# Performance work log

Measured on AMD Instinct MI355X. Metric: run time of the kernel, lower is better.

The kernel has to match this reference:

```python
import jax, jax.numpy as jnp
import numpy as np

B, S, D, H = 4, 2048, 512, 8
HD = D // H  # head_dim = 64


def setup_inputs() -> dict:
    key = jax.random.key(0)
    ks = jax.random.split(key, 6)
    s = 1.0 / np.sqrt(D)
    return {
        "value": jax.random.normal(ks[0], (B, S, D), jnp.float32),
        "key": jax.random.normal(ks[1], (B, S, D), jnp.float32),
        "query": jax.random.normal(ks[2], (B, S, D), jnp.float32),
        "Wv": jax.random.normal(ks[3], (D, D), jnp.float32) * s,
        "bv": jnp.zeros((D,), jnp.float32),
        "Wk": jax.random.normal(ks[4], (D, D), jnp.float32) * s,
        "bk": jnp.zeros((D,), jnp.float32),
        "Wq": jax.random.normal(ks[5], (D, D), jnp.float32) * s,
        "bq": jnp.zeros((D,), jnp.float32),
    }


def _heads(x):
    # [B,S,D] -> [B,H,S,hd]
    return x.reshape(B, S, H, HD).transpose(0, 2, 1, 3)


def reference(value, key, query, Wv, bv, Wk, bk, Wq, bq):
    v = _heads(value @ Wv.T + bv)
    k = _heads(key @ Wk.T + bk)
    q = _heads(query @ Wq.T + bq)
    scale = 1.0 / jnp.sqrt(jnp.asarray(HD, q.dtype))
    # two scaled-dot-product score maps, each [B,H,S,S]
    att_kq = jax.nn.softmax(jnp.einsum("bhqd,bhkd->bhqk", q, k) * scale, axis=-1)
    att_vq = jax.nn.softmax(jnp.einsum("bhqd,bhkd->bhqk", q, v) * scale, axis=-1)
    att_map = att_kq + att_vq
    fused = v + k  # [B,H,S,hd]
    attended = jnp.einsum("bhqk,bhkd->bhqd", att_map, fused)
    # elementwise multiply with q, reduce over the sequence (query) axis
    head_logits = jnp.sum(attended * q, axis=2)  # [B,H,hd]
    return head_logits.reshape(B, H * HD)
```

## Files before the change

kernel.cpp:

```cpp
#include <hip/hip_runtime.h>
#include <hip/hip_bf16.h>

#define Bq 4
#define Sq 2048
#define Dq 512
#define Hq 8
#define HDq 64

typedef __attribute__((ext_vector_type(8))) short short8;
typedef __attribute__((ext_vector_type(4))) float f32x4;

#if __has_builtin(__builtin_amdgcn_exp2f)
#define EXP2(x) __builtin_amdgcn_exp2f(x)
#else
#define EXP2(x) exp2f(x)
#endif

#define SCALE2 (0.125f * 1.44269504088896340736f)
#define INV_SCALE2 (5.545177444479562f)

__device__ __forceinline__ short bfs(float x) {
    __hip_bfloat16 h = __float2bfloat16(x);
    short r;
    __builtin_memcpy(&r, &h, 2);
    return r;
}

__device__ __forceinline__ short8 cvt8(float4 a, float4 b) {
    union { __hip_bfloat16 h[8]; short8 s; } u;
    u.h[0] = __float2bfloat16(a.x); u.h[1] = __float2bfloat16(a.y);
    u.h[2] = __float2bfloat16(a.z); u.h[3] = __float2bfloat16(a.w);
    u.h[4] = __float2bfloat16(b.x); u.h[5] = __float2bfloat16(b.y);
    u.h[6] = __float2bfloat16(b.z); u.h[7] = __float2bfloat16(b.w);
    return u.s;
}

__device__ __forceinline__ void gload16(const void* g, void* l) {
    __builtin_amdgcn_global_load_lds(
        (const __attribute__((address_space(1))) unsigned int*)g,
        (__attribute__((address_space(3))) unsigned int*)l, 16, 0, 0);
}

__global__ __launch_bounds__(256, 3)
void proj_kernel(const float* __restrict__ Xv, const float* __restrict__ Xk, const float* __restrict__ Xq,
                 const float* __restrict__ Wv, const float* __restrict__ Wk, const float* __restrict__ Wq,
                 const float* __restrict__ bv, const float* __restrict__ bk, const float* __restrict__ bq,
                 __hip_bfloat16* __restrict__ Ov, __hip_bfloat16* __restrict__ Ok, __hip_bfloat16* __restrict__ Oq) {
    __shared__ alignas(16) short As[128 * 64];
    __shared__ alignas(16) short Bs[128 * 64];

    const int z = blockIdx.z;
    const float* X   = (z == 0) ? Xv : (z == 1) ? Xk : Xq;
    const float* W   = (z == 0) ? Wv : (z == 1) ? Wk : Wq;
    const float* bia = (z == 0) ? bv : (z == 1) ? bk : bq;
    __hip_bfloat16* O = (z == 0) ? Ov : (z == 1) ? Ok : Oq;
    const float sc = (z == 2) ? SCALE2 : 1.0f;

    const int tid  = threadIdx.x;
    const int lane = tid & 63;
    const int w    = tid >> 6;
    const int wr   = w >> 1;
    const int wc   = w & 1;
    const int m0   = blockIdx.y * 128;
    const int n0   = blockIdx.x * 128;
    const int arow = lane & 15;
    const int ag   = lane >> 4;

    f32x4 acc[4][4];
    #pragma unroll
    for (int t = 0; t < 4; ++t)
        #pragma unroll
        for (int u = 0; u < 4; ++u) acc[t][u] = (f32x4){0.f, 0.f, 0.f, 0.f};

    for (int kk = 0; kk < Dq / 64; ++kk) {
        __syncthreads();
        #pragma unroll
        for (int p = 0; p < 4; ++p) {
            int id  = p * 256 + tid;
            int row = id >> 3;
            int c   = id & 7;
            int dst = row * 128 + ((c * 16) ^ ((row & 7) << 4));
            const float* ax = X + (size_t)(m0 + row) * Dq + kk * 64 + c * 8;
            const float* bx = W + (size_t)(n0 + row) * Dq + kk * 64 + c * 8;
            float4 a0 = *(const float4*)ax;
            float4 a1 = *(const float4*)(ax + 4);
            float4 b0 = *(const float4*)bx;
            float4 b1 = *(const float4*)(bx + 4);
            *(short8*)((char*)As + dst) = cvt8(a0, a1);
            *(short8*)((char*)Bs + dst) = cvt8(b0, b1);
        }
        __syncthreads();
        #pragma unroll
        for (int h = 0; h < 2; ++h) {
            short8 af[4], bf[4];
            #pragma unroll
            for (int t = 0; t < 4; ++t) {
                int ra = wr * 64 + t * 16 + arow;
                int rb = wc * 64 + t * 16 + arow;
                af[t] = *(const short8*)((const char*)As + ra * 128 + ((h * 64 + ag * 16) ^ ((ra & 7) << 4)));
                bf[t] = *(const short8*)((const char*)Bs + rb * 128 + ((h * 64 + ag * 16) ^ ((rb & 7) << 4)));
            }
            #pragma unroll
            for (int t = 0; t < 4; ++t)
                #pragma unroll
                for (int u = 0; u < 4; ++u)
                    acc[t][u] = __builtin_amdgcn_mfma_f32_16x16x32_bf16(af[t], bf[u], acc[t][u], 0, 0, 0);
        }
    }

    float biasv[4];
    #pragma unroll
    for (int u = 0; u < 4; ++u) biasv[u] = bia[n0 + wc * 64 + u * 16 + arow];

    #pragma unroll
    for (int t = 0; t < 4; ++t) {
        #pragma unroll
        for (int u = 0; u < 4; ++u) {
            #pragma unroll
            for (int r = 0; r < 4; ++r) {
                int m = m0 + wr * 64 + t * 16 + 4 * ag + r;
                int n = n0 + wc * 64 + u * 16 + arow;
                int b = m >> 11, s = m & 2047;
                int hh = n >> 6, hd = n & 63;
                O[((((size_t)b * Hq + hh) * Sq + s) << 6) + hd] =
                    __float2bfloat16((acc[t][u][r] + biasv[u]) * sc);
            }
        }
    }
}

__global__ __launch_bounds__(256)
void fuse_t_kernel(const __hip_bfloat16* __restrict__ Kh, const __hip_bfloat16* __restrict__ Vh,
                   __hip_bfloat16* __restrict__ Ft) {
    __shared__ float T[64][65];
    const int bh = blockIdx.x >> 5;
    const int st = blockIdx.x & 31;
    const int tid = threadIdx.x;

    #pragma unroll
    for (int p = 0; p < 2; ++p) {
        int idx = p * 256 + tid;
        int r = idx >> 3;
        int c = (idx & 7) * 8;
        size_t g = ((size_t)bh * Sq + st * 64 + r) * 64 + c;
        float4 k4 = *(const float4*)((const char*)Kh + g * 2);
        float4 v4 = *(const float4*)((const char*)Vh + g * 2);
        const __hip_bfloat16* kp = (const __hip_bfloat16*)&k4;
        const __hip_bfloat16* vp = (const __hip_bfloat16*)&v4;
        #pragma unroll
        for (int j = 0; j < 8; ++j)
            T[r][c + j] = __bfloat162float(kp[j]) + __bfloat162float(vp[j]);
    }
    __syncthreads();
    #pragma unroll
    for (int pp = 0; pp < 2; ++pp) {
        int idx = pp * 256 + tid;
        int d  = idx >> 3;
        int p8 = (idx & 7) * 8;
        alignas(16) __hip_bfloat16 tmp[8];
        #pragma unroll
        for (int j2 = 0; j2 < 8; ++j2) {
            int p = p8 + j2;
            int h  = p >> 5;
            int ag = (p >> 3) & 3;
            int j  = p & 7;
            int k  = 16 * (2 * (j >> 2) + h) + 4 * ag + (j & 3);
            tmp[j2] = __float2bfloat16(T[k][d]);
        }
        *(float4*)((char*)Ft + (((size_t)bh * 64 + d) * Sq + st * 64 + p8) * 2) = *(const float4*)tmp;
    }
}

__global__ __launch_bounds__(512, 4)
void attn_kernel(const __hip_bfloat16* __restrict__ Qh, const __hip_bfloat16* __restrict__ Kh,
                 const __hip_bfloat16* __restrict__ Vh, const __hip_bfloat16* __restrict__ Ft,
                 float* __restrict__ part) {
    __shared__ alignas(16) short Qs[128 * 64];
    __shared__ alignas(16) short Ks[64 * 64];
    __shared__ alignas(16) short Vs[64 * 64];
    __shared__ alignas(16) short Fs[64 * 64];
    __shared__ float part_s[8][64];

    const int tid  = threadIdx.x;
    const int lane = tid & 63;
    const int w    = tid >> 6;
    const int lb   = (blockIdx.x & 7) * 64 + (blockIdx.x >> 3);
    const int bh   = lb >> 4;
    const int s0   = (lb & 15) * 128;

    const char* Qbh = (const char*)(Qh + (size_t)bh * Sq * 64);
    const char* Kbh = (const char*)(Kh + (size_t)bh * Sq * 64);
    const char* Vbh = (const char*)(Vh + (size_t)bh * Sq * 64);
    const char* Fbh = (const char*)(Ft + (size_t)bh * 64 * Sq);

    #pragma unroll
    for (int p = 0; p < 2; ++p) {
        int idx = p * 512 + tid;
        int r = idx >> 3;
        int c = idx & 7;
        int swz = (r & 7) << 4;
        float4 q4 = *(const float4*)(Qbh + ((size_t)(s0 + r) * 64 + c * 8) * 2);
        *(float4*)((char*)Qs + r * 128 + ((c * 16) ^ swz)) = q4;
    }
    __syncthreads();

    const int arow = lane & 15;
    const int ag   = lane >> 4;
    const int aswz = (arow & 7) << 4;

    const int qrow = w * 16 + arow;
    short8 qa0 = *(const short8*)((const char*)Qs + qrow * 128 + ((16 * ag) ^ aswz));
    short8 qa1 = *(const short8*)((const char*)Qs + qrow * 128 + ((64 + 16 * ag) ^ aswz));

    f32x4 acc_k[4], acc_v[4];
    #pragma unroll
    for (int t = 0; t < 4; ++t) {
        acc_k[t] = (f32x4){0.f, 0.f, 0.f, 0.f};
        acc_v[t] = (f32x4){0.f, 0.f, 0.f, 0.f};
    }
    float lp_k = 0.f, lp_v = 0.f;

    const int sgr = w * 8 + (lane >> 3);
    const int scs = (lane & 7) ^ (sgr & 7);
    const size_t koff = ((size_t)sgr * 64 + scs * 8) * 2;
    char* ldsK = (char*)Ks + w * 1024;
    char* ldsV = (char*)Vs + w * 1024;
    char* ldsF = (char*)Fs + w * 1024;

    for (int ck = 0; ck < Sq / 64; ++ck) {
        const int kv0 = ck * 64;
        __syncthreads();
        gload16(Kbh + (size_t)kv0 * 128 + koff, ldsK);
        gload16(Vbh + (size_t)kv0 * 128 + koff, ldsV);
        gload16(Fbh + ((size_t)sgr * Sq + kv0 + scs * 8) * 2, ldsF);
        __syncthreads();

        f32x4 sk[4], sv[4];
        #pragma unroll
        for (int t = 0; t < 4; ++t) {
            sk[t] = (f32x4){0.f, 0.f, 0.f, 0.f};
            sv[t] = (f32x4){0.f, 0.f, 0.f, 0.f};
        }
        #pragma unroll
        for (int t = 0; t < 4; ++t) {
            int brow = t * 16 + arow;
            int bswz = (brow & 7) << 4;
            short8 kb0 = *(const short8*)((const char*)Ks + brow * 128 + ((16 * ag) ^ bswz));
            short8 kb1 = *(const short8*)((const char*)Ks + brow * 128 + ((64 + 16 * ag) ^ bswz));
            short8 vb0 = *(const short8*)((const char*)Vs + brow * 128 + ((16 * ag) ^ bswz));
            short8 vb1 = *(const short8*)((const char*)Vs + brow * 128 + ((64 + 16 * ag) ^ bswz));
            sk[t] = __builtin_amdgcn_mfma_f32_16x16x32_bf16(kb0, qa0, sk[t], 0, 0, 0);
            sk[t] = __builtin_amdgcn_mfma_f32_16x16x32_bf16(kb1, qa1, sk[t], 0, 0, 0);
            sv[t] = __builtin_amdgcn_mfma_f32_16x16x32_bf16(vb0, qa0, sv[t], 0, 0, 0);
            sv[t] = __builtin_amdgcn_mfma_f32_16x16x32_bf16(vb1, qa1, sv[t], 0, 0, 0);
        }

        short8 bpk[2], bpv[2];
        #pragma unroll
        for (int t = 0; t < 4; ++t) {
            #pragma unroll
            for (int r = 0; r < 4; ++r) {
                float ek = EXP2(sk[t][r]);
                float ev = EXP2(sv[t][r]);
                lp_k += ek; lp_v += ev;
                bpk[t & 1][4 * (t >> 1) + r] = bfs(ek);
                bpv[t & 1][4 * (t >> 1) + r] = bfs(ev);
            }
        }

        #pragma unroll
        for (int td = 0; td < 4; ++td) {
            int row = td * 16 + arow;
            int rswz = (row & 7) << 4;
            short8 fa0 = *(const short8*)((const char*)Fs + row * 128 + ((16 * ag) ^ rswz));
            short8 fa1 = *(const short8*)((const char*)Fs + row * 128 + ((64 + 16 * ag) ^ rswz));
            acc_k[td] = __builtin_amdgcn_mfma_f32_16x16x32_bf16(fa0, bpk[0], acc_k[td], 0, 0, 0);
            acc_k[td] = __builtin_amdgcn_mfma_f32_16x16x32_bf16(fa1, bpk[1], acc_k[td], 0, 0, 0);
            acc_v[td] = __builtin_amdgcn_mfma_f32_16x16x32_bf16(fa0, bpv[0], acc_v[td], 0, 0, 0);
            acc_v[td] = __builtin_amdgcn_mfma_f32_16x16x32_bf16(fa1, bpv[1], acc_v[td], 0, 0, 0);
        }
    }

    lp_k += __shfl_xor(lp_k, 16); lp_k += __shfl_xor(lp_k, 32);
    lp_v += __shfl_xor(lp_v, 16); lp_v += __shfl_xor(lp_v, 32);
    float ilk = INV_SCALE2 / lp_k;
    float ilv = INV_SCALE2 / lp_v;

    f32x4 c[4];
    #pragma unroll
    for (int td = 0; td < 4; ++td) {
        #pragma unroll
        for (int r = 0; r < 4; ++r) {
            int d = 16 * td + 4 * ag + r;
            int byte = 2 * d;
            float qv = __bfloat162float(*(const __hip_bfloat16*)(
                (const char*)Qs + qrow * 128 + (((byte & ~15) ^ ((qrow & 7) << 4)) | (byte & 15))));
            c[td][r] = (acc_k[td][r] * ilk + acc_v[td][r] * ilv) * qv;
        }
    }
    #pragma unroll
    for (int off = 1; off < 16; off <<= 1) {
        #pragma unroll
        for (int td = 0; td < 4; ++td) {
            #pragma unroll
            for (int r = 0; r < 4; ++r) c[td][r] += __shfl_xor(c[td][r], off);
        }
    }
    if (arow == 0) {
        #pragma unroll
        for (int td = 0; td < 4; ++td)
            #pragma unroll
            for (int r = 0; r < 4; ++r)
                part_s[w][16 * td + 4 * ag + r] = c[td][r];
    }
    __syncthreads();
    if (tid < 64) {
        float t = 0.f;
        #pragma unroll
        for (int r = 0; r < 8; ++r) t += part_s[r][tid];
        part[(size_t)lb * 64 + tid] = t;
    }
}

__global__ void reduce_kernel(const float* __restrict__ part, float* __restrict__ out) {
    int bh = blockIdx.x;
    int d  = threadIdx.x;
    float t = 0.f;
    for (int i = 0; i < 16; ++i)
        t += part[(size_t)(bh * 16 + i) * 64 + d];
    out[bh * 64 + d] = t;
}

extern "C" void kernel_launch(void* const* d_in, const int* in_sizes, int n_in,
                              void* d_out, int out_size, void* d_ws, size_t ws_size,
                              hipStream_t stream) {
    const float* value = (const float*)d_in[0];
    const float* key   = (const float*)d_in[1];
    const float* query = (const float*)d_in[2];
    const float* Wv    = (const float*)d_in[3];
    const float* bv    = (const float*)d_in[4];
    const float* Wk    = (const float*)d_in[5];
    const float* bk    = (const float*)d_in[6];
    const float* Wq    = (const float*)d_in[7];
    const float* bq    = (const float*)d_in[8];
    float* out = (float*)d_out;

    char* w = (char*)d_ws;
    __hip_bfloat16* Qh = (__hip_bfloat16*)(w);
    __hip_bfloat16* Kh = (__hip_bfloat16*)(w + (size_t)8  * 1024 * 1024);
    __hip_bfloat16* Vh = (__hip_bfloat16*)(w + (size_t)16 * 1024 * 1024);
    __hip_bfloat16* Ft = (__hip_bfloat16*)(w + (size_t)24 * 1024 * 1024);
    float*          part = (float*)      (w + (size_t)32 * 1024 * 1024);

    dim3 pg(Dq / 128, (Bq * Sq) / 128, 3);
    proj_kernel<<<pg, 256, 0, stream>>>(value, key, query, Wv, Wk, Wq, bv, bk, bq, Vh, Kh, Qh);

    fuse_t_kernel<<<1024, 256, 0, stream>>>(Kh, Vh, Ft);
    attn_kernel<<<512, 512, 0, stream>>>(Qh, Kh, Vh, Ft, part);
    reduce_kernel<<<32, 64, 0, stream>>>(part, out);
}
```

Before: 126.6 us.

## Double-buffer K/V/F LDS tiles to prefetch next chunk during compute

Splits the K, V and fused-F shared-memory tiles into two buffers. The first chunk is loaded before the loop, and each iteration issues the global-to-LDS loads for the next chunk before running the current chunk's MFMA and softmax work. This replaces the two barriers per iteration with a single barrier at the end, so load latency can overlap with compute. The cost is double the LDS for those tiles, which can reduce how many blocks fit per CU.

```diff
diff --git a/kernel.cpp b/kernel.cpp
--- a/kernel.cpp
+++ b/kernel.cpp
@@ -176,9 +176,9 @@
                  const __hip_bfloat16* __restrict__ Vh, const __hip_bfloat16* __restrict__ Ft,
                  float* __restrict__ part) {
     __shared__ alignas(16) short Qs[128 * 64];
-    __shared__ alignas(16) short Ks[64 * 64];
-    __shared__ alignas(16) short Vs[64 * 64];
-    __shared__ alignas(16) short Fs[64 * 64];
+    __shared__ alignas(16) short Ks[2][64 * 64];
+    __shared__ alignas(16) short Vs[2][64 * 64];
+    __shared__ alignas(16) short Fs[2][64 * 64];
     __shared__ float part_s[8][64];
 
     const int tid  = threadIdx.x;
@@ -202,6 +202,15 @@
         float4 q4 = *(const float4*)(Qbh + ((size_t)(s0 + r) * 64 + c * 8) * 2);
         *(float4*)((char*)Qs + r * 128 + ((c * 16) ^ swz)) = q4;
     }
+
+    const int sgr = w * 8 + (lane >> 3);
+    const int scs = (lane & 7) ^ (sgr & 7);
+    const size_t koff = ((size_t)sgr * 64 + scs * 8) * 2;
+    const int wb = w * 1024;
+
+    gload16(Kbh + koff, (char*)Ks[0] + wb);
+    gload16(Vbh + koff, (char*)Vs[0] + wb);
+    gload16(Fbh + ((size_t)sgr * Sq + scs * 8) * 2, (char*)Fs[0] + wb);
     __syncthreads();
 
     const int arow = lane & 15;
@@ -220,20 +229,15 @@
     }
     float lp_k = 0.f, lp_v = 0.f;
 
-    const int sgr = w * 8 + (lane >> 3);
-    const int scs = (lane & 7) ^ (sgr & 7);
-    const size_t koff = ((size_t)sgr * 64 + scs * 8) * 2;
-    char* ldsK = (char*)Ks + w * 1024;
-    char* ldsV = (char*)Vs + w * 1024;
-    char* ldsF = (char*)Fs + w * 1024;
-
     for (int ck = 0; ck < Sq / 64; ++ck) {
-        const int kv0 = ck * 64;
-        __syncthreads();
-        gload16(Kbh + (size_t)kv0 * 128 + koff, ldsK);
-        gload16(Vbh + (size_t)kv0 * 128 + koff, ldsV);
-        gload16(Fbh + ((size_t)sgr * Sq + kv0 + scs * 8) * 2, ldsF);
-        __syncthreads();
+        const int cb = ck & 1;
+        if (ck + 1 < Sq / 64) {
+            const int nb  = cb ^ 1;
+            const size_t kv1 = (size_t)(ck + 1) * 64;
+            gload16(Kbh + kv1 * 128 + koff, (char*)Ks[nb] + wb);
+            gload16(Vbh + kv1 * 128 + koff, (char*)Vs[nb] + wb);
+            gload16(Fbh + ((size_t)sgr * Sq + kv1 + scs * 8) * 2, (char*)Fs[nb] + wb);
+        }
 
         f32x4 sk[4], sv[4];
         #pragma unroll
@@ -245,10 +249,10 @@
         for (int t = 0; t < 4; ++t) {
             int brow = t * 16 + arow;
             int bswz = (brow & 7) << 4;
-            short8 kb0 = *(const short8*)((const char*)Ks + brow * 128 + ((16 * ag) ^ bswz));
-            short8 kb1 = *(const short8*)((const char*)Ks + brow * 128 + ((64 + 16 * ag) ^ bswz));
-            short8 vb0 = *(const short8*)((const char*)Vs + brow * 128 + ((16 * ag) ^ bswz));
-            short8 vb1 = *(const short8*)((const char*)Vs + brow * 128 + ((64 + 16 * ag) ^ bswz));
+            short8 kb0 = *(const short8*)((const char*)Ks[cb] + brow * 128 + ((16 * ag) ^ bswz));
+            short8 kb1 = *(const short8*)((const char*)Ks[cb] + brow * 128 + ((64 + 16 * ag) ^ bswz));
+            short8 vb0 = *(const short8*)((const char*)Vs[cb] + brow * 128 + ((16 * ag) ^ bswz));
+            short8 vb1 = *(const short8*)((const char*)Vs[cb] + brow * 128 + ((64 + 16 * ag) ^ bswz));
             sk[t] = __builtin_amdgcn_mfma_f32_16x16x32_bf16(kb0, qa0, sk[t], 0, 0, 0);
             sk[t] = __builtin_amdgcn_mfma_f32_16x16x32_bf16(kb1, qa1, sk[t], 0, 0, 0);
             sv[t] = __builtin_amdgcn_mfma_f32_16x16x32_bf16(vb0, qa0, sv[t], 0, 0, 0);
@@ -272,13 +276,15 @@
         for (int td = 0; td < 4; ++td) {
             int row = td * 16 + arow;
             int rswz = (row & 7) << 4;
-            short8 fa0 = *(const short8*)((const char*)Fs + row * 128 + ((16 * ag) ^ rswz));
-            short8 fa1 = *(const short8*)((const char*)Fs + row * 128 + ((64 + 16 * ag) ^ rswz));
+            short8 fa0 = *(const short8*)((const char*)Fs[cb] + row * 128 + ((16 * ag) ^ rswz));
+            short8 fa1 = *(const short8*)((const char*)Fs[cb] + row * 128 + ((64 + 16 * ag) ^ rswz));
             acc_k[td] = __builtin_amdgcn_mfma_f32_16x16x32_bf16(fa0, bpk[0], acc_k[td], 0, 0, 0);
             acc_k[td] = __builtin_amdgcn_mfma_f32_16x16x32_bf16(fa1, bpk[1], acc_k[td], 0, 0, 0);
             acc_v[td] = __builtin_amdgcn_mfma_f32_16x16x32_bf16(fa0, bpv[0], acc_v[td], 0, 0, 0);
             acc_v[td] = __builtin_amdgcn_mfma_f32_16x16x32_bf16(fa1, bpv[1], acc_v[td], 0, 0, 0);
         }
+
+        __syncthreads();
     }
 
     lp_k += __shfl_xor(lp_k, 16); lp_k += __shfl_xor(lp_k, 32);
```

Measured after the change: 127.4 us. About the same (+0.6%).

## Software-pipeline attention loop with double-buffered K/V and two query tiles per wave

Applied to the files above, without the earlier changes.

Restructures the attention kernel to 256 threads where each wave handles two 16-row query tiles, reusing each K/V LDS fragment twice. K/V are double-buffered in LDS and the QK^T of the next chunk is interleaved with exp and PV of the previous chunk. Q and the fused F operand are read straight from global memory instead of LDS, and softmax denominators are accumulated with MFMA against a ones vector. It also adds s_setprio hints around the MFMA bursts. The cost is more registers per thread, lower occupancy, and uncached global reads of F inside the loop.

```diff
diff --git a/kernel.cpp b/kernel.cpp
--- a/kernel.cpp
+++ b/kernel.cpp
@@ -6,6 +6,7 @@
 #define Dq 512
 #define Hq 8
 #define HDq 64
+#define NCHUNK 32
 
 typedef __attribute__((ext_vector_type(8))) short short8;
 typedef __attribute__((ext_vector_type(4))) float f32x4;
@@ -171,14 +172,12 @@
     }
 }
 
-__global__ __launch_bounds__(512, 4)
+__global__ __launch_bounds__(256, 2)
 void attn_kernel(const __hip_bfloat16* __restrict__ Qh, const __hip_bfloat16* __restrict__ Kh,
                  const __hip_bfloat16* __restrict__ Vh, const __hip_bfloat16* __restrict__ Ft,
                  float* __restrict__ part) {
-    __shared__ alignas(16) short Qs[128 * 64];
-    __shared__ alignas(16) short Ks[64 * 64];
-    __shared__ alignas(16) short Vs[64 * 64];
-    __shared__ alignas(16) short Fs[64 * 64];
+    __shared__ alignas(16) short Ks[2][64 * 64];
+    __shared__ alignas(16) short Vs[2][64 * 64];
     __shared__ float part_s[8][64];
 
     const int tid  = threadIdx.x;
@@ -193,125 +192,181 @@
     const char* Vbh = (const char*)(Vh + (size_t)bh * Sq * 64);
     const char* Fbh = (const char*)(Ft + (size_t)bh * 64 * Sq);
 
-    #pragma unroll
-    for (int p = 0; p < 2; ++p) {
-        int idx = p * 512 + tid;
-        int r = idx >> 3;
-        int c = idx & 7;
-        int swz = (r & 7) << 4;
-        float4 q4 = *(const float4*)(Qbh + ((size_t)(s0 + r) * 64 + c * 8) * 2);
-        *(float4*)((char*)Qs + r * 128 + ((c * 16) ^ swz)) = q4;
-    }
-    __syncthreads();
-
     const int arow = lane & 15;
     const int ag   = lane >> 4;
-    const int aswz = (arow & 7) << 4;
-
-    const int qrow = w * 16 + arow;
-    short8 qa0 = *(const short8*)((const char*)Qs + qrow * 128 + ((16 * ag) ^ aswz));
-    short8 qa1 = *(const short8*)((const char*)Qs + qrow * 128 + ((64 + 16 * ag) ^ aswz));
-
-    f32x4 acc_k[4], acc_v[4];
-    #pragma unroll
-    for (int t = 0; t < 4; ++t) {
-        acc_k[t] = (f32x4){0.f, 0.f, 0.f, 0.f};
-        acc_v[t] = (f32x4){0.f, 0.f, 0.f, 0.f};
-    }
-    float lp_k = 0.f, lp_v = 0.f;
-
-    const int sgr = w * 8 + (lane >> 3);
-    const int scs = (lane & 7) ^ (sgr & 7);
-    const size_t koff = ((size_t)sgr * 64 + scs * 8) * 2;
-    char* ldsK = (char*)Ks + w * 1024;
-    char* ldsV = (char*)Vs + w * 1024;
-    char* ldsF = (char*)Fs + w * 1024;
-
-    for (int ck = 0; ck < Sq / 64; ++ck) {
-        const int kv0 = ck * 64;
+
+    short8 qa[2][2];
+    #pragma unroll
+    for (int tile = 0; tile < 2; ++tile) {
+        int qrg = s0 + w * 32 + tile * 16 + arow;
+        qa[tile][0] = *(const short8*)(Qbh + ((size_t)qrg * 64 + 8 * ag) * 2);
+        qa[tile][1] = *(const short8*)(Qbh + ((size_t)qrg * 64 + 32 + 8 * ag) * 2);
+    }
+
+    short8 ones;
+    #pragma unroll
+    for (int j = 0; j < 8; ++j) ones[j] = (short)0x3F80;
+
+    f32x4 acc_k[2][4], acc_v[2][4];
+    f32x4 acc_lk[2], acc_lv[2];
+    #pragma unroll
+    for (int tile = 0; tile < 2; ++tile) {
+        #pragma unroll
+        for (int t = 0; t < 4; ++t) {
+            acc_k[tile][t] = (f32x4){0.f, 0.f, 0.f, 0.f};
+            acc_v[tile][t] = (f32x4){0.f, 0.f, 0.f, 0.f};
+        }
+        acc_lk[tile] = (f32x4){0.f, 0.f, 0.f, 0.f};
+        acc_lv[tile] = (f32x4){0.f, 0.f, 0.f, 0.f};
+    }
+
+    int sbyte[2];
+    size_t kof[2];
+    #pragma unroll
+    for (int p = 0; p < 2; ++p) {
+        int row = p * 32 + w * 8 + (lane >> 3);
+        int scs = (lane & 7) ^ (row & 7);
+        sbyte[p] = p * 4096 + w * 1024;
+        kof[p] = ((size_t)row * 64 + scs * 8) * 2;
+    }
+
+    const char* fbase[4];
+    #pragma unroll
+    for (int td = 0; td < 4; ++td)
+        fbase[td] = Fbh + (size_t)(td * 16 + arow) * Sq * 2 + 16 * ag;
+
+    f32x4 skA[2][4], svA[2][4], skB[2][4], svB[2][4];
+
+#define STAGE(CN) do { if ((CN) < NCHUNK) {                                    \
+    const size_t kv_ = (size_t)(CN) * 64;                                      \
+    char* kb_ = (char*)Ks[(CN) & 1];                                           \
+    char* vb_ = (char*)Vs[(CN) & 1];                                           \
+    _Pragma("unroll")                                                          \
+    for (int p_ = 0; p_ < 2; ++p_) {                                           \
+        gload16(Kbh + kv_ * 128 + kof[p_], kb_ + sbyte[p_]);                   \
+        gload16(Vbh + kv_ * 128 + kof[p_], vb_ + sbyte[p_]);                   \
+    } } } while (0)
+
+#define QKM(CK, SK, SV) do {                                                   \
+    const char* kbase_ = (const char*)Ks[(CK) & 1];                            \
+    const char* vbase_ = (const char*)Vs[(CK) & 1];                            \
+    _Pragma("unroll")                                                          \
+    for (int tl_ = 0; tl_ < 2; ++tl_)                                          \
+        _Pragma("unroll")                                                      \
+        for (int t_ = 0; t_ < 4; ++t_) {                                       \
+            SK[tl_][t_] = (f32x4){0.f, 0.f, 0.f, 0.f};                         \
+            SV[tl_][t_] = (f32x4){0.f, 0.f, 0.f, 0.f};                         \
+        }                                                                      \
+    __builtin_amdgcn_s_setprio(1);                                             \
+    _Pragma("unroll")                                                          \
+    for (int t_ = 0; t_ < 4; ++t_) {                                           \
+        int brow_ = t_ * 16 + arow;                                            \
+        int bswz_ = (brow_ & 7) << 4;                                          \
+        short8 kb0_ = *(const short8*)(kbase_ + brow_ * 128 + ((16 * ag) ^ bswz_));        \
+        short8 kb1_ = *(const short8*)(kbase_ + brow_ * 128 + ((64 + 16 * ag) ^ bswz_));   \
+        short8 vb0_ = *(const short8*)(vbase_ + brow_ * 128 + ((16 * ag) ^ bswz_));        \
+        short8 vb1_ = *(const short8*)(vbase_ + brow_ * 128 + ((64 + 16 * ag) ^ bswz_));   \
+        _Pragma("unroll")                                                      \
+        for (int tl_ = 0; tl_ < 2; ++tl_) {                                    \
+            SK[tl_][t_] = __builtin_amdgcn_mfma_f32_16x16x32_bf16(kb0_, qa[tl_][0], SK[tl_][t_], 0, 0, 0); \
+            SK[tl_][t_] = __builtin_amdgcn_mfma_f32_16x16x32_bf16(kb1_, qa[tl_][1], SK[tl_][t_], 0, 0, 0); \
+            SV[tl_][t_] = __builtin_amdgcn_mfma_f32_16x16x32_bf16(vb0_, qa[tl_][0], SV[tl_][t_], 0, 0, 0); \
+            SV[tl_][t_] = __builtin_amdgcn_mfma_f32_16x16x32_bf16(vb1_, qa[tl_][1], SV[tl_][t_], 0, 0, 0); \
+        }                                                                      \
+    }                                                                          \
+    __builtin_amdgcn_s_setprio(0);                                             \
+} while (0)
+
+#define EXPPV(CKP, SK, SV) do {                                                \
+    short8 bpk_[2][2], bpv_[2][2];                                             \
+    _Pragma("unroll")                                                          \
+    for (int tl_ = 0; tl_ < 2; ++tl_)                                          \
+        _Pragma("unroll")                                                      \
+        for (int t_ = 0; t_ < 4; ++t_)                                         \
+            _Pragma("unroll")                                                  \
+            for (int r_ = 0; r_ < 4; ++r_) {                                   \
+                bpk_[tl_][t_ & 1][4 * (t_ >> 1) + r_] = bfs(EXP2(SK[tl_][t_][r_])); \
+                bpv_[tl_][t_ & 1][4 * (t_ >> 1) + r_] = bfs(EXP2(SV[tl_][t_][r_])); \
+            }                                                                  \
+    const size_t fco_ = (size_t)(CKP) * 128;                                   \
+    __builtin_amdgcn_s_setprio(1);                                             \
+    _Pragma("unroll")                                                          \
+    for (int td_ = 0; td_ < 4; ++td_) {                                        \
+        short8 fa0_ = *(const short8*)(fbase[td_] + fco_);                     \
+        short8 fa1_ = *(const short8*)(fbase[td_] + fco_ + 64);                \
+        _Pragma("unroll")                                                      \
+        for (int tl_ = 0; tl_ < 2; ++tl_) {                                    \
+            acc_k[tl_][td_] = __builtin_amdgcn_mfma_f32_16x16x32_bf16(fa0_, bpk_[tl_][0], acc_k[tl_][td_], 0, 0, 0); \
+            acc_k[tl_][td_] = __builtin_amdgcn_mfma_f32_16x16x32_bf16(fa1_, bpk_[tl_][1], acc_k[tl_][td_], 0, 0, 0); \
+            acc_v[tl_][td_] = __builtin_amdgcn_mfma_f32_16x16x32_bf16(fa0_, bpv_[tl_][0], acc_v[tl_][td_], 0, 0, 0); \
+            acc_v[tl_][td_] = __builtin_amdgcn_mfma_f32_16x16x32_bf16(fa1_, bpv_[tl_][1], acc_v[tl_][td_], 0, 0, 0); \
+        }                                                                      \
+    }                                                                          \
+    _Pragma("unroll")                                                          \
+    for (int tl_ = 0; tl_ < 2; ++tl_) {                                        \
+        acc_lk[tl_] = __builtin_amdgcn_mfma_f32_16x16x32_bf16(ones, bpk_[tl_][0], acc_lk[tl_], 0, 0, 0); \
+        acc_lk[tl_] = __builtin_amdgcn_mfma_f32_16x16x32_bf16(ones, bpk_[tl_][1], acc_lk[tl_], 0, 0, 0); \
+        acc_lv[tl_] = __builtin_amdgcn_mfma_f32_16x16x32_bf16(ones, bpv_[tl_][0], acc_lv[tl_], 0, 0, 0); \
+        acc_lv[tl_] = __builtin_amdgcn_mfma_f32_16x16x32_bf16(ones, bpv_[tl_][1], acc_lv[tl_], 0, 0, 0); \
+    }                                                                          \
+    __builtin_amdgcn_s_setprio(0);                                             \
+} while (0)
+
+    STAGE(0);
+    __syncthreads();
+    STAGE(1);
+    QKM(0, skA, svA);
+    for (int c = 1; c < NCHUNK - 1; c += 2) {
         __syncthreads();
-        gload16(Kbh + (size_t)kv0 * 128 + koff, ldsK);
-        gload16(Vbh + (size_t)kv0 * 128 + koff, ldsV);
-        gload16(Fbh + ((size_t)sgr * Sq + kv0 + scs * 8) * 2, ldsF);
+        STAGE(c + 1);
+        QKM(c, skB, svB);
+        EXPPV(c - 1, skA, svA);
         __syncthreads();
-
-        f32x4 sk[4], sv[4];
-        #pragma unroll
-        for (int t = 0; t < 4; ++t) {
-            sk[t] = (f32x4){0.f, 0.f, 0.f, 0.f};
-            sv[t] = (f32x4){0.f, 0.f, 0.f, 0.f};
-        }
-        #pragma unroll
-        for (int t = 0; t < 4; ++t) {
-            int brow = t * 16 + arow;
-            int bswz = (brow & 7) << 4;
-            short8 kb0 = *(const short8*)((const char*)Ks + brow * 128 + ((16 * ag) ^ bswz));
-            short8 kb1 = *(const short8*)((const char*)Ks + brow * 128 + ((64 + 16 * ag) ^ bswz));
-            short8 vb0 = *(const short8*)((const char*)Vs + brow * 128 + ((16 * ag) ^ bswz));
-            short8 vb1 = *(const short8*)((const char*)Vs + brow * 128 + ((64 + 16 * ag) ^ bswz));
-            sk[t] = __builtin_amdgcn_mfma_f32_16x16x32_bf16(kb0, qa0, sk[t], 0, 0, 0);
-            sk[t] = __builtin_amdgcn_mfma_f32_16x16x32_bf16(kb1, qa1, sk[t], 0, 0, 0);
-            sv[t] = __builtin_amdgcn_mfma_f32_16x16x32_bf16(vb0, qa0, sv[t], 0, 0, 0);
-            sv[t] = __builtin_amdgcn_mfma_f32_16x16x32_bf16(vb1, qa1, sv[t], 0, 0, 0);
-        }
-
-        short8 bpk[2], bpv[2];
-        #pragma unroll
-        for (int t = 0; t < 4; ++t) {
+        STAGE(c + 2);
+        QKM(c + 1, skA, svA);
+        EXPPV(c, skB, svB);
+    }
+    __syncthreads();
+    QKM(NCHUNK - 1, skB, svB);
+    EXPPV(NCHUNK - 2, skA, svA);
+    EXPPV(NCHUNK - 1, skB, svB);
+
+#undef STAGE
+#undef QKM
+#undef EXPPV
+
+    #pragma unroll
+    for (int tile = 0; tile < 2; ++tile) {
+        float ilk = INV_SCALE2 / acc_lk[tile][0];
+        float ilv = INV_SCALE2 / acc_lv[tile][0];
+
+        int qrg = s0 + w * 32 + tile * 16 + arow;
+        f32x4 c[4];
+        #pragma unroll
+        for (int td = 0; td < 4; ++td) {
             #pragma unroll
             for (int r = 0; r < 4; ++r) {
-                float ek = EXP2(sk[t][r]);
-                float ev = EXP2(sv[t][r]);
-                lp_k += ek; lp_v += ev;
-                bpk[t & 1][4 * (t >> 1) + r] = bfs(ek);
-                bpv[t & 1][4 * (t >> 1) + r] = bfs(ev);
+                int d = 16 * td + 4 * ag + r;
+                float qv = __bfloat162float(*(const __hip_bfloat16*)(
+                    Qbh + ((size_t)qrg * 64 + d) * 2));
+                c[td][r] = (acc_k[tile][td][r] * ilk + acc_v[tile][td][r] * ilv) * qv;
             }
         }
-
-        #pragma unroll
-        for (int td = 0; td < 4; ++td) {
-            int row = td * 16 + arow;
-            int rswz = (row & 7) << 4;
-            short8 fa0 = *(const short8*)((const char*)Fs + row * 128 + ((16 * ag) ^ rswz));
-            short8 fa1 = *(const short8*)((const char*)Fs + row * 128 + ((64 + 16 * ag) ^ rswz));
-            acc_k[td] = __builtin_amdgcn_mfma_f32_16x16x32_bf16(fa0, bpk[0], acc_k[td], 0, 0, 0);
-            acc_k[td] = __builtin_amdgcn_mfma_f32_16x16x32_bf16(fa1, bpk[1], acc_k[td], 0, 0, 0);
-            acc_v[td] = __builtin_amdgcn_mfma_f32_16x16x32_bf16(fa0, bpv[0], acc_v[td], 0, 0, 0);
-            acc_v[td] = __builtin_amdgcn_mfma_f32_16x16x32_bf16(fa1, bpv[1], acc_v[td], 0, 0, 0);
-        }
-    }
-
-    lp_k += __shfl_xor(lp_k, 16); lp_k += __shfl_xor(lp_k, 32);
-    lp_v += __shfl_xor(lp_v, 16); lp_v += __shfl_xor(lp_v, 32);
-    float ilk = INV_SCALE2 / lp_k;
-    float ilv = INV_SCALE2 / lp_v;
-
-    f32x4 c[4];
-    #pragma unroll
-    for (int td = 0; td < 4; ++td) {
-        #pragma unroll
-        for (int r = 0; r < 4; ++r) {
-            int d = 16 * td + 4 * ag + r;
-            int byte = 2 * d;
-            float qv = __bfloat162float(*(const __hip_bfloat16*)(
-                (const char*)Qs + qrow * 128 + (((byte & ~15) ^ ((qrow & 7) << 4)) | (byte & 15))));
-            c[td][r] = (acc_k[td][r] * ilk + acc_v[td][r] * ilv) * qv;
-        }
-    }
-    #pragma unroll
-    for (int off = 1; off < 16; off <<= 1) {
-        #pragma unroll
-        for (int td = 0; td < 4; ++td) {
-            #pragma unroll
-            for (int r = 0; r < 4; ++r) c[td][r] += __shfl_xor(c[td][r], off);
-        }
-    }
-    if (arow == 0) {
-        #pragma unroll
-        for (int td = 0; td < 4; ++td)
-            #pragma unroll
-            for (int r = 0; r < 4; ++r)
-                part_s[w][16 * td + 4 * ag + r] = c[td][r];
+        #pragma unroll
+        for (int off = 1; off < 16; off <<= 1) {
+            #pragma unroll
+            for (int td = 0; td < 4; ++td) {
+                #pragma unroll
+                for (int r = 0; r < 4; ++r) c[td][r] += __shfl_xor(c[td][r], off);
+            }
+        }
+        if (arow == 0) {
+            #pragma unroll
+            for (int td = 0; td < 4; ++td)
+                #pragma unroll
+                for (int r = 0; r < 4; ++r)
+                    part_s[w * 2 + tile][16 * td + 4 * ag + r] = c[td][r];
+        }
     }
     __syncthreads();
     if (tid < 64) {
@@ -356,6 +411,6 @@
     proj_kernel<<<pg, 256, 0, stream>>>(value, key, query, Wv, Wk, Wq, bv, bk, bq, Vh, Kh, Qh);
 
     fuse_t_kernel<<<1024, 256, 0, stream>>>(Kh, Vh, Ft);
-    attn_kernel<<<512, 512, 0, stream>>>(Qh, Kh, Vh, Ft, part);
+    attn_kernel<<<512, 256, 0, stream>>>(Qh, Kh, Vh, Ft, part);
     reduce_kernel<<<32, 64, 0, stream>>>(part, out);
 }
```

New measurement: 212.0 us. 67.5% more time.
